# Kernel optimization log

Hardware: AMD Instinct MI355X
Metric: run time of the kernel (lower is better)

Reference implementation:

```python
import jax, jax.numpy as jnp
import numpy as np

N_NODES = 50000
N_EDGES = 300000
DIM = 256
ALPHA = 0.1  # residual mixing with initial features, as passed in forward


def gcn_layer(x0, x, edge_idx, W):
    """One GraphConvolution call: mean neighbor aggregation over the edge
    list, GCNII-style residual mix with initial features x0, then linear."""
    src, dst = edge_idx[0], edge_idx[1]
    msgs = x[src]  # [E, D] gather
    agg = jax.ops.segment_sum(msgs, dst, num_segments=x.shape[0])
    deg = jax.ops.segment_sum(jnp.ones((src.shape[0],), x.dtype), dst,
                              num_segments=x.shape[0])
    agg = agg / jnp.maximum(deg, 1.0)[:, None]
    h = ALPHA * x0 + (1.0 - ALPHA) * agg
    return h @ W


def setup_inputs() -> dict:
    key = jax.random.key(0)
    k1, k2, k3 = jax.random.split(key, 3)
    x = jax.random.normal(k1, (N_NODES, DIM), dtype=jnp.float32)
    edge_idx = jax.random.randint(k2, (2, N_EDGES), 0, N_NODES, dtype=jnp.int64)
    W = jax.random.normal(k3, (DIM, DIM), dtype=jnp.float32) / np.sqrt(DIM)
    return {"drug_cell_pair_feature": x, "edge_idx": edge_idx, "W": W}


def reference(drug_cell_pair_feature, edge_idx, W):
    x0 = drug_cell_pair_feature
    out = jax.nn.relu(gcn_layer(x0, x0, edge_idx, W))
    for _ in range(4):  # 4 more identical calls, always mixing with x0
        out = jax.nn.relu(gcn_layer(x0, out, edge_idx, W))
    return out
```

## Files before the change

kernel.cpp:

```cpp
#include <hip/hip_runtime.h>

#define DIM 256
#define ELL_W 32

typedef __attribute__((ext_vector_type(8))) short short8;
typedef __attribute__((ext_vector_type(8))) unsigned short u16x8;
typedef __attribute__((ext_vector_type(4))) float f32x4;

__device__ __forceinline__ unsigned short f32_to_bf16(float x) {
    unsigned int u = __float_as_uint(x);
    unsigned int r = u + 0x7FFFu + ((u >> 16) & 1u);
    return (unsigned short)(r >> 16);
}
__device__ __forceinline__ float bf16_to_f32(unsigned short h) {
    return __uint_as_float(((unsigned int)h) << 16);
}

__device__ __forceinline__ void load_lds16(const void* g, void* l) {
    __builtin_amdgcn_global_load_lds(
        (const __attribute__((address_space(1))) unsigned int*)g,
        (__attribute__((address_space(3))) unsigned int*)l, 16, 0, 0);
}

__global__ void fillprep_kernel(const int* __restrict__ src, const int* __restrict__ dst,
                                int E, int* __restrict__ cursor, int* __restrict__ ell,
                                const float* __restrict__ W, unsigned short* __restrict__ Wt,
                                const float* __restrict__ x0, unsigned short* __restrict__ x0b,
                                int n4, int nbE) {
    int b = blockIdx.x;
    if (b < nbE) {
        int e = b * 256 + threadIdx.x;
        if (e < E) {
            int d = dst[e];
            int pos = atomicAdd(&cursor[d], 1);
            if (pos < ELL_W) ell[d * ELL_W + pos] = src[e];
        }
    } else if (b < nbE + DIM) {
        int k = b - nbE, n = threadIdx.x;
        Wt[n * DIM + k] = f32_to_bf16(W[k * DIM + n]);
    } else {
        int i = (b - nbE - DIM) * 256 + threadIdx.x;
        if (i < n4) {
            float4 v = ((const float4*)x0)[i];
            ushort4 o;
            o.x = f32_to_bf16(v.x); o.y = f32_to_bf16(v.y);
            o.z = f32_to_bf16(v.z); o.w = f32_to_bf16(v.w);
            ((ushort4*)x0b)[i] = o;
        }
    }
}

__global__ __launch_bounds__(256) void aggregate_kernel(
    const unsigned short* __restrict__ xh, const unsigned short* __restrict__ x0b,
    const int* __restrict__ deg, const int* __restrict__ ell,
    unsigned short* __restrict__ h, int N)
{
    int node = blockIdx.x * 4 + (threadIdx.x >> 6);
    if (node >= N) return;
    const int lane = threadIdx.x & 63;
    const int half = lane >> 5;
    const int c    = (lane & 31) * 8;

    const int dg = deg[node];
    const int ec = min(dg, ELL_W);
    const int* __restrict__ lst = ell + node * ELL_W;

    const float dscale = 0.9f / (float)max(dg, 1);
    const u16x8 xv = *(const u16x8*)(x0b + (size_t)node * DIM + c);

    float a[8];
    #pragma unroll
    for (int j = 0; j < 8; j++) a[j] = 0.f;

    int e = 0;
    for (; e + 4 <= ec; e += 4) {
        int s0 = lst[e + half];
        int s1 = lst[e + 2 + half];
        u16x8 v0 = *(const u16x8*)(xh + (size_t)s0 * DIM + c);
        u16x8 v1 = *(const u16x8*)(xh + (size_t)s1 * DIM + c);
        #pragma unroll
        for (int j = 0; j < 8; j++) a[j] += bf16_to_f32(v0[j]) + bf16_to_f32(v1[j]);
    }
    if (e + 2 <= ec) {
        int s0 = lst[e + half];
        u16x8 v0 = *(const u16x8*)(xh + (size_t)s0 * DIM + c);
        #pragma unroll
        for (int j = 0; j < 8; j++) a[j] += bf16_to_f32(v0[j]);
        e += 2;
    }
    if (e < ec && half == 0) {
        int s0 = lst[e];
        u16x8 v0 = *(const u16x8*)(xh + (size_t)s0 * DIM + c);
        #pragma unroll
        for (int j = 0; j < 8; j++) a[j] += bf16_to_f32(v0[j]);
    }

    #pragma unroll
    for (int j = 0; j < 8; j++) a[j] += __shfl_xor(a[j], 32);

    if (half == 0) {
        u16x8 o;
        #pragma unroll
        for (int j = 0; j < 8; j++)
            o[j] = f32_to_bf16(0.1f * bf16_to_f32(xv[j]) + dscale * a[j]);
        *(u16x8*)(h + (size_t)node * DIM + c) = o;
    }
}

template <bool LAST>
__global__ __launch_bounds__(256) void gemm_kernel(
    const unsigned short* __restrict__ h, const unsigned short* __restrict__ Wt,
    float* __restrict__ out_f32, unsigned short* __restrict__ out_bf16, int N)
{
    __shared__ unsigned short As[3][128 * 32];
    __shared__ unsigned short Bs[3][128 * 32];

    const int t    = threadIdx.x;
    const int w    = t >> 6;
    const int lane = t & 63;
    const int lm   = lane & 15;
    const int q    = lane >> 4;
    const int wm   = w >> 1, wn = w & 1;
    const int m0   = blockIdx.x * 128;
    const int n0   = blockIdx.y * 128;

    const int sr = t >> 2;
    const int sg = ((t & 3) ^ ((t >> 3) & 3)) * 8;
    const int xr = (lm >> 1) & 3;

    f32x4 acc[4][4];
    #pragma unroll
    for (int mi = 0; mi < 4; mi++)
        #pragma unroll
        for (int ni = 0; ni < 4; ni++)
            acc[mi][ni] = (f32x4){0.f, 0.f, 0.f, 0.f};

    auto stage = [&](int kb, int buf) {
        #pragma unroll
        for (int half = 0; half < 2; half++) {
            int r = half * 64 + sr;
            int ldso = (half * 256 + t) * 8;
            load_lds16(h  + (size_t)(m0 + r) * DIM + kb + sg, &As[buf][ldso]);
            load_lds16(Wt + (size_t)(n0 + r) * DIM + kb + sg, &Bs[buf][ldso]);
        }
    };

    stage(0, 0);
    stage(32, 1);

    #pragma unroll
    for (int ks = 0; ks < 8; ks++) {
        const int p = ks % 3;
        if (ks < 7) asm volatile("s_waitcnt vmcnt(4)" ::: "memory");
        else        asm volatile("s_waitcnt vmcnt(0)" ::: "memory");
        __builtin_amdgcn_s_barrier();

        short8 a[4];
        #pragma unroll
        for (int mi = 0; mi < 4; mi++) {
            int row = wm * 64 + mi * 16 + lm;
            a[mi] = *(const short8*)&As[p][row * 32 + (q ^ xr) * 8];
        }

        if (ks < 6) stage((ks + 2) * 32, (ks + 2) % 3);

        #pragma unroll
        for (int ni = 0; ni < 4; ni++) {
            int row = wn * 64 + ni * 16 + lm;
            short8 b = *(const short8*)&Bs[p][row * 32 + (q ^ xr) * 8];
            #pragma unroll
            for (int mi = 0; mi < 4; mi++)
                acc[mi][ni] = __builtin_amdgcn_mfma_f32_16x16x32_bf16(a[mi], b, acc[mi][ni], 0, 0, 0);
        }
    }

    #pragma unroll
    for (int mi = 0; mi < 4; mi++) {
        const int rowb = m0 + wm * 64 + mi * 16 + q * 4;
        #pragma unroll
        for (int ni = 0; ni < 4; ni++) {
            const int col = n0 + wn * 64 + ni * 16 + lm;
            #pragma unroll
            for (int r = 0; r < 4; r++) {
                int row = rowb + r;
                if (row < N) {
                    float v = fmaxf(acc[mi][ni][r], 0.0f);
                    if (LAST) out_f32[(size_t)row * DIM + col] = v;
                    else      out_bf16[(size_t)row * DIM + col] = f32_to_bf16(v);
                }
            }
        }
    }
}

extern "C" void kernel_launch(void* const* d_in, const int* in_sizes, int n_in,
                              void* d_out, int out_size, void* d_ws, size_t ws_size,
                              hipStream_t stream) {
    const float* x0  = (const float*)d_in[0];
    const int*   ei  = (const int*)d_in[1];
    const float* W   = (const float*)d_in[2];
    float*       out = (float*)d_out;

    const int N = in_sizes[0] / DIM;
    const int E = in_sizes[1] / 2;
    const int N_pad = (N + 127) & ~127;
    const int* src = ei;
    const int* dst = ei + E;

    char* ws = (char*)d_ws;
    size_t off = 0;
    auto alloc = [&](size_t bytes) { char* p = ws + off; off += (bytes + 15) & ~size_t(15); return p; };
    unsigned short* h       = (unsigned short*)alloc((size_t)N_pad * DIM * 2);
    unsigned short* act     = (unsigned short*)alloc((size_t)N_pad * DIM * 2);
    unsigned short* x0b     = (unsigned short*)alloc((size_t)N_pad * DIM * 2);
    unsigned short* Wt      = (unsigned short*)alloc((size_t)DIM * DIM * 2);
    int*   cursor   = (int*)  alloc((size_t)N * 4);
    int*   ell      = (int*)  alloc((size_t)N * ELL_W * 4);

    const int nbE = (E + 255) / 256;
    const int n4 = N * DIM / 4;
    hipMemsetAsync(cursor, 0, (size_t)N * 4, stream);
    fillprep_kernel<<<nbE + DIM + (n4 + 255) / 256, 256, 0, stream>>>(
        src, dst, E, cursor, ell, W, Wt, x0, x0b, n4, nbE);

    dim3 ggrid(N_pad / 128, 2);
    for (int layer = 0; layer < 5; layer++) {
        const unsigned short* gsrc = (layer == 0) ? x0b : act;
        aggregate_kernel<<<(N + 3) / 4, 256, 0, stream>>>(gsrc, x0b, cursor, ell, h, N);
        if (layer == 4)
            gemm_kernel<true><<<ggrid, 256, 0, stream>>>(h, Wt, out, nullptr, N);
        else
            gemm_kernel<false><<<ggrid, 256, 0, stream>>>(h, Wt, nullptr, act, N);
    }
}
```

Before: 362.2 us.

## Fuse neighbor aggregation and GEMM into a single per-layer kernel

Measured after the change: 379.8 us. 1.05x slower.

```diff
diff --git a/kernel.cpp b/kernel.cpp
--- a/kernel.cpp
+++ b/kernel.cpp
@@ -2,6 +2,7 @@
 
 #define DIM 256
 #define ELL_W 32
+#define TM 32
 
 typedef __attribute__((ext_vector_type(8))) short short8;
 typedef __attribute__((ext_vector_type(8))) unsigned short u16x8;
@@ -14,12 +15,6 @@
 }
 __device__ __forceinline__ float bf16_to_f32(unsigned short h) {
     return __uint_as_float(((unsigned int)h) << 16);
-}
-
-__device__ __forceinline__ void load_lds16(const void* g, void* l) {
-    __builtin_amdgcn_global_load_lds(
-        (const __attribute__((address_space(1))) unsigned int*)g,
-        (__attribute__((address_space(3))) unsigned int*)l, 16, 0, 0);
 }
 
 __global__ void fillprep_kernel(const int* __restrict__ src, const int* __restrict__ dst,
@@ -50,136 +45,112 @@
     }
 }
 
-__global__ __launch_bounds__(256) void aggregate_kernel(
+template <bool LAST>
+__global__ __launch_bounds__(256, 5) void layer_kernel(
     const unsigned short* __restrict__ xh, const unsigned short* __restrict__ x0b,
+    const unsigned short* __restrict__ Wt,
     const int* __restrict__ deg, const int* __restrict__ ell,
-    unsigned short* __restrict__ h, int N)
-{
-    int node = blockIdx.x * 4 + (threadIdx.x >> 6);
-    if (node >= N) return;
-    const int lane = threadIdx.x & 63;
-    const int half = lane >> 5;
-    const int c    = (lane & 31) * 8;
-
-    const int dg = deg[node];
-    const int ec = min(dg, ELL_W);
-    const int* __restrict__ lst = ell + node * ELL_W;
-
-    const float dscale = 0.9f / (float)max(dg, 1);
-    const u16x8 xv = *(const u16x8*)(x0b + (size_t)node * DIM + c);
-
-    float a[8];
-    #pragma unroll
-    for (int j = 0; j < 8; j++) a[j] = 0.f;
-
-    int e = 0;
-    for (; e + 4 <= ec; e += 4) {
-        int s0 = lst[e + half];
-        int s1 = lst[e + 2 + half];
-        u16x8 v0 = *(const u16x8*)(xh + (size_t)s0 * DIM + c);
-        u16x8 v1 = *(const u16x8*)(xh + (size_t)s1 * DIM + c);
-        #pragma unroll
-        for (int j = 0; j < 8; j++) a[j] += bf16_to_f32(v0[j]) + bf16_to_f32(v1[j]);
-    }
-    if (e + 2 <= ec) {
-        int s0 = lst[e + half];
-        u16x8 v0 = *(const u16x8*)(xh + (size_t)s0 * DIM + c);
-        #pragma unroll
-        for (int j = 0; j < 8; j++) a[j] += bf16_to_f32(v0[j]);
-        e += 2;
-    }
-    if (e < ec && half == 0) {
-        int s0 = lst[e];
-        u16x8 v0 = *(const u16x8*)(xh + (size_t)s0 * DIM + c);
-        #pragma unroll
-        for (int j = 0; j < 8; j++) a[j] += bf16_to_f32(v0[j]);
-    }
-
-    #pragma unroll
-    for (int j = 0; j < 8; j++) a[j] += __shfl_xor(a[j], 32);
-
-    if (half == 0) {
-        u16x8 o;
-        #pragma unroll
-        for (int j = 0; j < 8; j++)
-            o[j] = f32_to_bf16(0.1f * bf16_to_f32(xv[j]) + dscale * a[j]);
-        *(u16x8*)(h + (size_t)node * DIM + c) = o;
-    }
-}
-
-template <bool LAST>
-__global__ __launch_bounds__(256) void gemm_kernel(
-    const unsigned short* __restrict__ h, const unsigned short* __restrict__ Wt,
     float* __restrict__ out_f32, unsigned short* __restrict__ out_bf16, int N)
 {
-    __shared__ unsigned short As[3][128 * 32];
-    __shared__ unsigned short Bs[3][128 * 32];
+    __shared__ unsigned short hs[TM * 256];
 
     const int t    = threadIdx.x;
     const int w    = t >> 6;
     const int lane = t & 63;
-    const int lm   = lane & 15;
-    const int q    = lane >> 4;
-    const int wm   = w >> 1, wn = w & 1;
-    const int m0   = blockIdx.x * 128;
-    const int n0   = blockIdx.y * 128;
-
-    const int sr = t >> 2;
-    const int sg = ((t & 3) ^ ((t >> 3) & 3)) * 8;
-    const int xr = (lm >> 1) & 3;
-
-    f32x4 acc[4][4];
-    #pragma unroll
-    for (int mi = 0; mi < 4; mi++)
+    const int half = lane >> 5;
+    const int hw   = (w << 1) + half;
+    const int cl   = lane & 31;
+    const int c    = cl * 8;
+    const int m0   = blockIdx.x * TM;
+
+    #pragma unroll
+    for (int i = 0; i < TM / 8; i++) {
+        const int lrow = hw * (TM / 8) + i;
+        const int node = m0 + lrow;
+        unsigned short* dp = &hs[lrow * 256 + (cl ^ (lrow & 7)) * 8];
+        if (node < N) {
+            const int dg = deg[node];
+            const int ec = min(dg, ELL_W);
+            const int* __restrict__ lst = ell + node * ELL_W;
+            const float dscale = 0.9f / (float)max(dg, 1);
+            const u16x8 xv = *(const u16x8*)(x0b + (size_t)node * DIM + c);
+            float a[8];
+            #pragma unroll
+            for (int j = 0; j < 8; j++) a[j] = 0.f;
+            int e = 0;
+            for (; e + 4 <= ec; e += 4) {
+                int s0 = lst[e], s1 = lst[e + 1], s2 = lst[e + 2], s3 = lst[e + 3];
+                u16x8 v0 = *(const u16x8*)(xh + (size_t)s0 * DIM + c);
+                u16x8 v1 = *(const u16x8*)(xh + (size_t)s1 * DIM + c);
+                u16x8 v2 = *(const u16x8*)(xh + (size_t)s2 * DIM + c);
+                u16x8 v3 = *(const u16x8*)(xh + (size_t)s3 * DIM + c);
+                #pragma unroll
+                for (int j = 0; j < 8; j++)
+                    a[j] += (bf16_to_f32(v0[j]) + bf16_to_f32(v1[j]))
+                          + (bf16_to_f32(v2[j]) + bf16_to_f32(v3[j]));
+            }
+            if (e + 2 <= ec) {
+                int s0 = lst[e], s1 = lst[e + 1];
+                u16x8 v0 = *(const u16x8*)(xh + (size_t)s0 * DIM + c);
+                u16x8 v1 = *(const u16x8*)(xh + (size_t)s1 * DIM + c);
+                #pragma unroll
+                for (int j = 0; j < 8; j++)
+                    a[j] += bf16_to_f32(v0[j]) + bf16_to_f32(v1[j]);
+                e += 2;
+            }
+            if (e < ec) {
+                int s0 = lst[e];
+                u16x8 v0 = *(const u16x8*)(xh + (size_t)s0 * DIM + c);
+                #pragma unroll
+                for (int j = 0; j < 8; j++) a[j] += bf16_to_f32(v0[j]);
+            }
+            u16x8 o;
+            #pragma unroll
+            for (int j = 0; j < 8; j++)
+                o[j] = f32_to_bf16(0.1f * bf16_to_f32(xv[j]) + dscale * a[j]);
+            *(u16x8*)dp = o;
+        } else {
+            u16x8 z;
+            #pragma unroll
+            for (int j = 0; j < 8; j++) z[j] = 0;
+            *(u16x8*)dp = z;
+        }
+    }
+    __syncthreads();
+
+    const int lm = lane & 15, q = lane >> 4;
+    f32x4 acc[TM / 16][4];
+    #pragma unroll
+    for (int mi = 0; mi < TM / 16; mi++)
         #pragma unroll
         for (int ni = 0; ni < 4; ni++)
             acc[mi][ni] = (f32x4){0.f, 0.f, 0.f, 0.f};
 
-    auto stage = [&](int kb, int buf) {
-        #pragma unroll
-        for (int half = 0; half < 2; half++) {
-            int r = half * 64 + sr;
-            int ldso = (half * 256 + t) * 8;
-            load_lds16(h  + (size_t)(m0 + r) * DIM + kb + sg, &As[buf][ldso]);
-            load_lds16(Wt + (size_t)(n0 + r) * DIM + kb + sg, &Bs[buf][ldso]);
-        }
-    };
-
-    stage(0, 0);
-    stage(32, 1);
-
     #pragma unroll
     for (int ks = 0; ks < 8; ks++) {
-        const int p = ks % 3;
-        if (ks < 7) asm volatile("s_waitcnt vmcnt(4)" ::: "memory");
-        else        asm volatile("s_waitcnt vmcnt(0)" ::: "memory");
-        __builtin_amdgcn_s_barrier();
-
-        short8 a[4];
-        #pragma unroll
-        for (int mi = 0; mi < 4; mi++) {
-            int row = wm * 64 + mi * 16 + lm;
-            a[mi] = *(const short8*)&As[p][row * 32 + (q ^ xr) * 8];
-        }
-
-        if (ks < 6) stage((ks + 2) * 32, (ks + 2) % 3);
-
+        short8 a[TM / 16];
+        #pragma unroll
+        for (int mi = 0; mi < TM / 16; mi++) {
+            int row = mi * 16 + lm;
+            int ch = (ks * 4 + q) ^ (row & 7);
+            a[mi] = *(const short8*)&hs[row * 256 + ch * 8];
+        }
         #pragma unroll
         for (int ni = 0; ni < 4; ni++) {
-            int row = wn * 64 + ni * 16 + lm;
-            short8 b = *(const short8*)&Bs[p][row * 32 + (q ^ xr) * 8];
-            #pragma unroll
-            for (int mi = 0; mi < 4; mi++)
+            int brow = w * 64 + ni * 16 + lm;
+            short8 b = *(const short8*)(Wt + (size_t)brow * DIM + ks * 32 + q * 8);
+            #pragma unroll
+            for (int mi = 0; mi < TM / 16; mi++)
                 acc[mi][ni] = __builtin_amdgcn_mfma_f32_16x16x32_bf16(a[mi], b, acc[mi][ni], 0, 0, 0);
         }
     }
 
     #pragma unroll
-    for (int mi = 0; mi < 4; mi++) {
-        const int rowb = m0 + wm * 64 + mi * 16 + q * 4;
+    for (int mi = 0; mi < TM / 16; mi++) {
+        const int rowb = m0 + mi * 16 + q * 4;
         #pragma unroll
         for (int ni = 0; ni < 4; ni++) {
-            const int col = n0 + wn * 64 + ni * 16 + lm;
+            const int col = w * 64 + ni * 16 + lm;
             #pragma unroll
             for (int r = 0; r < 4; r++) {
                 int row = rowb + r;
@@ -210,8 +181,8 @@
     char* ws = (char*)d_ws;
     size_t off = 0;
     auto alloc = [&](size_t bytes) { char* p = ws + off; off += (bytes + 15) & ~size_t(15); return p; };
-    unsigned short* h       = (unsigned short*)alloc((size_t)N_pad * DIM * 2);
-    unsigned short* act     = (unsigned short*)alloc((size_t)N_pad * DIM * 2);
+    unsigned short* act0    = (unsigned short*)alloc((size_t)N_pad * DIM * 2);
+    unsigned short* act1    = (unsigned short*)alloc((size_t)N_pad * DIM * 2);
     unsigned short* x0b     = (unsigned short*)alloc((size_t)N_pad * DIM * 2);
     unsigned short* Wt      = (unsigned short*)alloc((size_t)DIM * DIM * 2);
     int*   cursor   = (int*)  alloc((size_t)N * 4);
@@ -223,13 +194,17 @@
     fillprep_kernel<<<nbE + DIM + (n4 + 255) / 256, 256, 0, stream>>>(
         src, dst, E, cursor, ell, W, Wt, x0, x0b, n4, nbE);
 
-    dim3 ggrid(N_pad / 128, 2);
+    const int nbt = (N + TM - 1) / TM;
+    const unsigned short* gsrc = x0b;
+    unsigned short* gdst = act0;
     for (int layer = 0; layer < 5; layer++) {
-        const unsigned short* gsrc = (layer == 0) ? x0b : act;
-        aggregate_kernel<<<(N + 3) / 4, 256, 0, stream>>>(gsrc, x0b, cursor, ell, h, N);
         if (layer == 4)
-            gemm_kernel<true><<<ggrid, 256, 0, stream>>>(h, Wt, out, nullptr, N);
+            layer_kernel<true><<<nbt, 256, 0, stream>>>(gsrc, x0b, Wt, cursor, ell,
+                                                        out, nullptr, N);
         else
-            gemm_kernel<false><<<ggrid, 256, 0, stream>>>(h, Wt, nullptr, act, N);
-    }
-}
+            layer_kernel<false><<<nbt, 256, 0, stream>>>(gsrc, x0b, Wt, cursor, ell,
+                                                         nullptr, gdst, N);
+        gsrc = gdst;
+        gdst = (gdst == act0) ? act1 : act0;
+    }
+}
```
